# Optimization experiments

Hardware: AMD Instinct MI355X
Metric: run time of the kernel (lower is better)

The kernel has to match this reference:

```python
import jax, jax.numpy as jnp
from jax import lax
import jax.scipy.linalg as jsl
import numpy as np

R, N_MONTE, N_X = 8192, 64, 32


def _spd(a, n_x):
    # A @ A^T / n_x + I  -> well-conditioned SPD
    eye = jnp.eye(n_x, dtype=a.dtype)
    return jnp.einsum('...ij,...kj->...ik', a, a) / n_x + eye


def setup_inputs() -> dict:
    key = jax.random.key(0)
    k1, k2, k3, k4, k5 = jax.random.split(key, 5)
    x_hessian_diags = _spd(jax.random.normal(k1, (R, N_X, N_X), jnp.float32) * 0.5, N_X)
    x_grads = jax.random.normal(k2, (R, 1, N_X), jnp.float32) * 0.1
    x_trans_mat = jax.random.normal(k3, (N_X, N_X), jnp.float32) * (0.5 / np.sqrt(N_X))
    x_trans_prec = jnp.eye(N_X, dtype=jnp.float32)  # as in _compute_eta_loss_2
    x_init_prec = _spd(jax.random.normal(k4, (N_X, N_X), jnp.float32) * 0.5, N_X)
    epsx = jax.random.normal(k5, (R, N_MONTE, N_X), jnp.float32)
    return {
        'x_hessian_diags': x_hessian_diags,
        'x_grads': x_grads,
        'x_trans_mat': x_trans_mat,
        'x_trans_prec': x_trans_prec,
        'x_init_prec': x_init_prec,
        'epsx': epsx,
    }


def _cholesky_update(x_hessian_diags, x_grads, x_trans_mat, x_trans_prec, x_init_prec, epsx):
    r, n_monte, n_x = epsx.shape
    # A @ P @ A^T, constant across steps
    apat = x_trans_mat @ x_trans_prec @ x_trans_mat.T
    ap = x_trans_mat @ x_trans_prec
    # ms: 1 for all but the last step (last step has no successor coupling)
    ms = jnp.concatenate([jnp.ones(r - 1, x_hessian_diags.dtype), jnp.zeros(1, x_hessian_diags.dtype)])

    def fwd_step(carry, elem):
        pred_prec, off, u = carry  # [n_x,n_x], [n_x,n_x], [1,n_x]
        hess, grad, m = elem
        # block Cholesky diagonal factor
        chol = jnp.linalg.cholesky(pred_prec + hess + m * apat)
        # forward substitution for the mean rhs
        u = jsl.solve_triangular(chol, (grad - u @ off.T).T, lower=True).T
        # off-diagonal Cholesky block
        off = jsl.solve_triangular(chol, -ap, lower=True).T
        pred_prec = x_trans_prec - off @ off.T
        return (pred_prec, off, u), (chol, off, u)

    init = (x_init_prec, jnp.zeros((n_x, n_x), epsx.dtype), jnp.zeros((1, n_x), epsx.dtype))
    _, (chols, offs, us) = lax.scan(fwd_step, init, (x_hessian_diags, x_grads, ms))

    # backward substitution: smoothed mean (col 0) + posterior samples (cols 1:)
    gs = jnp.concatenate([us, epsx], axis=1)  # [R, 1+n_monte, n_x]

    def bwd_step(vw, elem):
        chol, off, g = elem
        vw = jsl.solve_triangular(chol.T, (g - vw @ off).T, lower=False).T
        return vw, vw

    _, vws = lax.scan(bwd_step, jnp.zeros((n_monte + 1, n_x), epsx.dtype), (chols, offs, gs), reverse=True)
    vs, ws = vws[:, :1], vws[:, 1:]
    return chols, offs, vs, ws


def reference(x_hessian_diags, x_grads, x_trans_mat, x_trans_prec, x_init_prec, epsx):
    _, _, vs, ws = _cholesky_update(x_hessian_diags, x_grads, x_trans_mat, x_trans_prec, x_init_prec, epsx)
    # x_tilde = vs + ws as consumed by _compute_eta_loss_2 (broadcast over n_monte)
    return vs + ws  # [R, n_monte, n_x]
```

## Files before the change

kernel.cpp:

```cpp
#include <hip/hip_runtime.h>
#include <hip/hip_bf16.h>

#define R_TOT 8192
#define NX 32
#define NM 64
#define STRD 33
#define VSTRD 36
#define OPSTRD 36
#define WARMF 8
#define WARMB 8
#define CHUNKF 4
#define CHUNKB 16

#define PIDX(k) ((((k) & 1) << 4) | ((k) >> 1))

__device__ inline void wsync() { asm volatile("s_waitcnt lgkmcnt(0)" ::: "memory"); }

__device__ inline float rdlane(float v, int l) {
  return __uint_as_float(__builtin_amdgcn_readlane(__float_as_uint(v), l));
}

__device__ inline unsigned f2bf(float x) {
  unsigned u = __float_as_uint(x);
  return (u + 0x7fffu + ((u >> 16) & 1u)) >> 16;
}

__device__ inline void st16(float* g, const float* v) {
  float4* p = reinterpret_cast<float4*>(g);
  p[0] = make_float4(v[0], v[1], v[2], v[3]);
  p[1] = make_float4(v[4], v[5], v[6], v[7]);
  p[2] = make_float4(v[8], v[9], v[10], v[11]);
  p[3] = make_float4(v[12], v[13], v[14], v[15]);
}
__device__ inline void st16(__hip_bfloat16* g, const float* v) {
  unsigned w[8];
  #pragma unroll
  for (int q = 0; q < 8; ++q)
    w[q] = (f2bf(v[2*q+1]) << 16) | f2bf(v[2*q]);
  uint4* p = reinterpret_cast<uint4*>(g);
  p[0] = make_uint4(w[0], w[1], w[2], w[3]);
  p[1] = make_uint4(w[4], w[5], w[6], w[7]);
}

__device__ inline void ld4(float* v, const float* g) {
  float4 a = *reinterpret_cast<const float4*>(g);
  v[0] = a.x; v[1] = a.y; v[2] = a.z; v[3] = a.w;
}
__device__ inline void ld4(float* v, const __hip_bfloat16* g) {
  uint2 a = *reinterpret_cast<const uint2*>(g);
  v[0] = __uint_as_float(a.x << 16);
  v[1] = __uint_as_float(a.x & 0xffff0000u);
  v[2] = __uint_as_float(a.y << 16);
  v[3] = __uint_as_float(a.y & 0xffff0000u);
}

__global__ __launch_bounds__(64) void precomp_kernel(
    const float* __restrict__ A, const float* __restrict__ P,
    float* __restrict__ apG, float* __restrict__ apatG)
{
  __shared__ float As[NX*STRD], Ps[NX*STRD], aps[NX*STRD];
  const int t = threadIdx.x;
  for (int e = t; e < NX*NX; e += 64) {
    int i = e >> 5, j = e & 31;
    As[i*STRD+j] = A[e];
    Ps[i*STRD+j] = P[e];
  }
  wsync();
  for (int e = t; e < NX*NX; e += 64) {
    int i = e >> 5, j = e & 31;
    float s = 0.f;
    for (int k = 0; k < NX; ++k) s += As[i*STRD+k] * Ps[k*STRD+j];
    aps[i*STRD+j] = s;
    apG[e] = s;
  }
  wsync();
  for (int e = t; e < NX*NX; e += 64) {
    int i = e >> 5, j = e & 31;
    float s = 0.f;
    for (int k = 0; k < NX; ++k) s += aps[i*STRD+k] * As[j*STRD+k];
    apatG[e] = s;
  }
}

template<typename ST>
__global__ __launch_bounds__(64, 2) void fwd_kernel(
    const float* __restrict__ hessAll, const float* __restrict__ gradAll,
    const float* __restrict__ apG, const float* __restrict__ apatG,
    const float* __restrict__ P, const float* __restrict__ initP,
    ST* __restrict__ offOut, ST* __restrict__ xOut, float* __restrict__ uOut)
{
  __shared__ float apP[NX*32], smx[NX*STRD], offP[NX*OPSTRD];
  __shared__ float uv[NX], tv[NX];
  const int t = threadIdx.x;
  const int lane = t & 31, half = t >> 5;
  const int pl = PIDX(lane);
  const int c = blockIdx.x;
  const int r0 = c * CHUNKF, r1 = r0 + CHUNKF;

  float PsR[16], apatR[16], predR[16], hessR[16];
  float gradR;

  const int cl = 16*(lane & 1) + (lane >> 1);
  #pragma unroll
  for (int m = 0; m < 16; ++m) {
    int e = t + 64*m;
    apP[(half + 2*m)*32 + cl] = apG[e];
    PsR[m]   = P[e];
    apatR[m] = apatG[e];
  }
  for (int e = t; e < NX*OPSTRD; e += 64) offP[e] = 0.f;
  wsync();

  int rstart = r0 - WARMF;
  if (rstart < 0) rstart = 0;
  const bool exact = (rstart == 0);

  #pragma unroll
  for (int m = 0; m < 16; ++m)
    predR[m] = exact ? initP[t + 64*m] : PsR[m];
  if (t < NX) uv[t] = 0.f;
  wsync();

  {
    const float* hess = hessAll + (size_t)rstart * (NX*NX);
    #pragma unroll
    for (int m = 0; m < 16; ++m) hessR[m] = hess[t + 64*m];
    gradR = gradAll[(size_t)rstart * NX + lane];
  }

  for (int r = rstart; r < r1; ++r) {
    const bool last = (r == R_TOT-1);
    #pragma unroll
    for (int m = 0; m < 16; ++m) {
      float v = predR[m] + hessR[m];
      if (!last) v += apatR[m];
      smx[(half + 2*m)*STRD + lane] = v;
    }
    wsync();
    if (r + 1 < r1) {
      const float* hn = hessAll + (size_t)(r+1) * (NX*NX);
      #pragma unroll
      for (int m = 0; m < 16; ++m) hessR[m] = hn[t + 64*m];
    }
    float row[NX];
    #pragma unroll
    for (int k = 0; k < NX; ++k) row[k] = smx[lane*STRD + k];
    #pragma unroll
    for (int j = 0; j < NX-1; ++j) {
      float invd = __builtin_amdgcn_rcpf(rdlane(row[j], j));
      float f = (lane > j) ? row[j] * invd : 0.f;
      #pragma unroll
      for (int cc = j+1; cc < NX; ++cc)
        row[cc] = fmaf(-f, rdlane(row[cc], j), row[cc]);
    }
    float zc[NX];
    #pragma unroll
    for (int i = 0; i < NX; ++i) {
      float d_i = rdlane(row[i], i);
      float di = __builtin_amdgcn_rcpf(d_i);
      float s = 0.f;
      #pragma unroll
      for (int k = 0; k < i; ++k) s = fmaf(rdlane(row[k], i), zc[k], s);
      zc[i] = (i == lane) ? di : -di * s;
    }
    #pragma unroll
    for (int i = 0; i < NX; ++i)
      zc[i] *= __builtin_amdgcn_sqrtf(rdlane(row[i], i));
    if (t < NX) {
      #pragma unroll
      for (int i = 0; i < NX; ++i) smx[i*STRD + t] = zc[i];
      if (r >= r0) {
        ST* xp = xOut + (size_t)r * (NX*NX) + t*NX;
        st16(xp, zc);
        st16(xp + 16, zc + 16);
      }
    }
    wsync();
    if (t < NX) {
      float s = gradR;
      #pragma unroll 4
      for (int m = 0; m < NX; ++m) s -= uv[m] * offP[m*OPSTRD + pl];
      tv[t] = s;
    }
    wsync();
    float unew = 0.f;
    if (t < NX) {
      float s = 0.f;
      #pragma unroll 4
      for (int k = 0; k < NX; ++k) s += tv[k] * smx[t*STRD+k];
      unew = s;
    }
    wsync();
    if (t < NX) {
      uv[t] = unew;
      if (r >= r0) uOut[(size_t)r*NX + t] = unew;
    }
    if (r + 1 < r1) gradR = gradAll[(size_t)(r+1) * NX + lane];
    wsync();
    {
      float offR[16];
      #pragma unroll
      for (int m = 0; m < 16; ++m) offR[m] = 0.f;
      #pragma unroll
      for (int k = 0; k < NX; ++k) {
        float xv = smx[lane*STRD + k];
        const float4* apv = reinterpret_cast<const float4*>(&apP[k*32 + 16*half]);
        float4 a0 = apv[0], a1 = apv[1], a2 = apv[2], a3 = apv[3];
        offR[0]  = fmaf(-xv, a0.x, offR[0]);  offR[1]  = fmaf(-xv, a0.y, offR[1]);
        offR[2]  = fmaf(-xv, a0.z, offR[2]);  offR[3]  = fmaf(-xv, a0.w, offR[3]);
        offR[4]  = fmaf(-xv, a1.x, offR[4]);  offR[5]  = fmaf(-xv, a1.y, offR[5]);
        offR[6]  = fmaf(-xv, a1.z, offR[6]);  offR[7]  = fmaf(-xv, a1.w, offR[7]);
        offR[8]  = fmaf(-xv, a2.x, offR[8]);  offR[9]  = fmaf(-xv, a2.y, offR[9]);
        offR[10] = fmaf(-xv, a2.z, offR[10]); offR[11] = fmaf(-xv, a2.w, offR[11]);
        offR[12] = fmaf(-xv, a3.x, offR[12]); offR[13] = fmaf(-xv, a3.y, offR[13]);
        offR[14] = fmaf(-xv, a3.z, offR[14]); offR[15] = fmaf(-xv, a3.w, offR[15]);
      }
      float4* opw = reinterpret_cast<float4*>(&offP[lane*OPSTRD + 16*half]);
      opw[0] = make_float4(offR[0],  offR[1],  offR[2],  offR[3]);
      opw[1] = make_float4(offR[4],  offR[5],  offR[6],  offR[7]);
      opw[2] = make_float4(offR[8],  offR[9],  offR[10], offR[11]);
      opw[3] = make_float4(offR[12], offR[13], offR[14], offR[15]);
      if (r >= r0)
        st16(offOut + (size_t)r * (NX*NX) + lane*NX + 16*half, offR);
    }
    wsync();
    #pragma unroll
    for (int m = 0; m < 16; ++m) predR[m] = PsR[m];
    #pragma unroll
    for (int k = 0; k < NX; ++k) {
      float fj = offP[k*OPSTRD + pl];
      const float4* ov = reinterpret_cast<const float4*>(&offP[k*OPSTRD + 16*half]);
      float4 o0 = ov[0], o1 = ov[1], o2 = ov[2], o3 = ov[3];
      predR[0]  -= o0.x*fj; predR[1]  -= o0.y*fj; predR[2]  -= o0.z*fj; predR[3]  -= o0.w*fj;
      predR[4]  -= o1.x*fj; predR[5]  -= o1.y*fj; predR[6]  -= o1.z*fj; predR[7]  -= o1.w*fj;
      predR[8]  -= o2.x*fj; predR[9]  -= o2.y*fj; predR[10] -= o2.z*fj; predR[11] -= o2.w*fj;
      predR[12] -= o3.x*fj; predR[13] -= o3.y*fj; predR[14] -= o3.z*fj; predR[15] -= o3.w*fj;
    }
    wsync();
  }
}

template<typename ST>
__global__ __launch_bounds__(256, 4) void bwd_kernel(
    const ST* __restrict__ offIn, const ST* __restrict__ xIn, const float* __restrict__ uIn,
    const float* __restrict__ epsx, float* __restrict__ outp)
{
  __shared__ float vw[(NM+1)*VSTRD], bb[(NM+1)*VSTRD], off[NX*STRD], xi[NX*STRD];
  const int t = threadIdx.x;
  const int lane = t & 31, grp = t >> 5;
  const int col = t >> 3, sg = t & 7;
  const int c = blockIdx.x;
  const int r0 = c * CHUNKB, r1 = r0 + CHUNKB;
  int rstart = r1 + WARMB; if (rstart > R_TOT) rstart = R_TOT;
  const bool has64 = (grp == 0);

  for (int e = t; e < (NM+1)*VSTRD; e += 256) vw[e] = 0.f;

  float ov[4], xv[4], gR[9];
  {
    int r = rstart - 1;
    size_t sb = (size_t)r * (NX*NX) + col*NX + 4*sg;
    ld4(ov, offIn + sb);
    ld4(xv, xIn + sb);
    const float* eps_r = epsx + (size_t)r * (NM*NX);
    const float* u_r   = uIn + (size_t)r * NX;
    #pragma unroll
    for (int m = 0; m < 8; ++m) {
      int i = grp + 8*m;
      gR[m] = (i == 0) ? u_r[lane] : eps_r[(i-1)*NX + lane];
    }
    gR[8] = has64 ? eps_r[63*NX + lane] : 0.f;
  }
  __syncthreads();

  for (int r = rstart - 1; r >= r0; --r) {
    float acc[9];
    #pragma unroll
    for (int m = 0; m < 9; ++m) acc[m] = gR[m];
    #pragma unroll
    for (int q = 0; q < 4; ++q) {
      int s = 4*sg + q;
      int io = ((s >> 4) & 1) | ((s & 15) << 1);
      off[io*STRD + col] = ov[q];
      xi[s*STRD + col]   = xv[q];
    }
    __syncthreads();
    if (r > r0) {
      size_t sb = (size_t)(r-1) * (NX*NX) + col*NX + 4*sg;
      ld4(ov, offIn + sb);
      ld4(xv, xIn + sb);
      const float* eps_n = epsx + (size_t)(r-1) * (NM*NX);
      const float* u_n   = uIn + (size_t)(r-1) * NX;
      #pragma unroll
      for (int m = 0; m < 8; ++m) {
        int i = grp + 8*m;
        gR[m] = (i == 0) ? u_n[lane] : eps_n[(i-1)*NX + lane];
      }
      if (has64) gR[8] = eps_n[63*NX + lane];
    }
    {
      float fo[NX];
      #pragma unroll
      for (int k = 0; k < NX; ++k) fo[k] = off[k*STRD + lane];
      #pragma unroll
      for (int m = 0; m < 8; ++m) {
        const float4* vr = reinterpret_cast<const float4*>(&vw[(grp + 8*m)*VSTRD]);
        #pragma unroll
        for (int q = 0; q < 8; ++q) {
          float4 v4 = vr[q];
          acc[m] -= v4.x*fo[4*q] + v4.y*fo[4*q+1] + v4.z*fo[4*q+2] + v4.w*fo[4*q+3];
        }
      }
      if (has64) {
        const float4* vr = reinterpret_cast<const float4*>(&vw[64*VSTRD]);
        #pragma unroll
        for (int q = 0; q < 8; ++q) {
          float4 v4 = vr[q];
          acc[8] -= v4.x*fo[4*q] + v4.y*fo[4*q+1] + v4.z*fo[4*q+2] + v4.w*fo[4*q+3];
        }
      }
    }
    #pragma unroll
    for (int m = 0; m < 8; ++m) bb[(grp + 8*m)*VSTRD + lane] = acc[m];
    if (has64) bb[64*VSTRD + lane] = acc[8];
    __syncthreads();
    float vacc[9];
    #pragma unroll
    for (int m = 0; m < 9; ++m) vacc[m] = 0.f;
    {
      float fx[NX];
      #pragma unroll
      for (int k = 0; k < NX; ++k) fx[k] = xi[k*STRD + lane];
      #pragma unroll
      for (int m = 0; m < 8; ++m) {
        const float4* br = reinterpret_cast<const float4*>(&bb[(grp + 8*m)*VSTRD]);
        #pragma unroll
        for (int q = 0; q < 8; ++q) {
          float4 b4 = br[q];
          vacc[m] += b4.x*fx[4*q] + b4.y*fx[4*q+1] + b4.z*fx[4*q+2] + b4.w*fx[4*q+3];
        }
      }
      if (has64) {
        const float4* br = reinterpret_cast<const float4*>(&bb[64*VSTRD]);
        #pragma unroll
        for (int q = 0; q < 8; ++q) {
          float4 b4 = br[q];
          vacc[8] += b4.x*fx[4*q] + b4.y*fx[4*q+1] + b4.z*fx[4*q+2] + b4.w*fx[4*q+3];
        }
      }
    }
    #pragma unroll
    for (int m = 0; m < 8; ++m) vw[(grp + 8*m)*VSTRD + lane] = vacc[m];
    if (has64) vw[64*VSTRD + lane] = vacc[8];
    __syncthreads();
    if (r < r1) {
      float v0 = vw[lane];
      float* out_r = outp + (size_t)r * (NM*NX);
      #pragma unroll
      for (int m = 0; m < 8; ++m)
        out_r[(grp + 8*m)*NX + lane] = vw[(grp + 8*m + 1)*VSTRD + lane] + v0;
    }
  }
}

extern "C" void kernel_launch(void* const* d_in, const int* in_sizes, int n_in,
                              void* d_out, int out_size, void* d_ws, size_t ws_size,
                              hipStream_t stream) {
  const float* hess  = (const float*)d_in[0];
  const float* grads = (const float*)d_in[1];
  const float* A     = (const float*)d_in[2];
  const float* P     = (const float*)d_in[3];
  const float* initP = (const float*)d_in[4];
  const float* epsx  = (const float*)d_in[5];
  float* outp = (float*)d_out;

  const size_t mats = (size_t)R_TOT * NX * NX;
  const size_t uN   = (size_t)R_TOT * NX;
  const size_t needF32 = 2ull * mats * sizeof(float) + uN * sizeof(float) + 2048 * sizeof(float);

  if (ws_size >= needF32) {
    float* offS  = (float*)d_ws;
    float* xS    = offS + mats;
    float* uS    = xS + mats;
    float* apG   = uS + uN;
    float* apatG = apG + 1024;
    precomp_kernel<<<dim3(1), dim3(64), 0, stream>>>(A, P, apG, apatG);
    fwd_kernel<float><<<dim3(R_TOT/CHUNKF), dim3(64), 0, stream>>>(
        hess, grads, apG, apatG, P, initP, offS, xS, uS);
    bwd_kernel<float><<<dim3(R_TOT/CHUNKB), dim3(256), 0, stream>>>(
        offS, xS, uS, epsx, outp);
  } else {
    __hip_bfloat16* offS = (__hip_bfloat16*)d_ws;
    __hip_bfloat16* xS   = offS + mats;
    float* uS            = (float*)(xS + mats);
    float* apG           = uS + uN;
    float* apatG         = apG + 1024;
    precomp_kernel<<<dim3(1), dim3(64), 0, stream>>>(A, P, apG, apatG);
    fwd_kernel<__hip_bfloat16><<<dim3(R_TOT/CHUNKF), dim3(64), 0, stream>>>(
        hess, grads, apG, apatG, P, initP, offS, xS, uS);
    bwd_kernel<__hip_bfloat16><<<dim3(R_TOT/CHUNKB), dim3(256), 0, stream>>>(
        offS, xS, uS, epsx, outp);
  }
}
```

Baseline: 470.6 us.

## Compute inverse Cholesky factor directly via elimination on identity rows

Replaces the two-phase approach (in-register LDL-style elimination of the matrix, then a separate triangular inversion) with a single sweep that builds the inverse factor row by row. Each step recomputes a pivot row as a dot product of the working rows with the original matrix columns, then eliminates. The output is stored transposed, and the backward kernel's indexing for xi is adjusted to match. The loops are kept rolled (unroll 1) and split so the first half only updates 16 columns, trading more readlane dot products per step for less code and lower register pressure.

```diff
diff --git a/kernel.cpp b/kernel.cpp
--- a/kernel.cpp
+++ b/kernel.cpp
@@ -142,37 +142,50 @@
       #pragma unroll
       for (int m = 0; m < 16; ++m) hessR[m] = hn[t + 64*m];
     }
-    float row[NX];
-    #pragma unroll
-    for (int k = 0; k < NX; ++k) row[k] = smx[lane*STRD + k];
-    #pragma unroll
-    for (int j = 0; j < NX-1; ++j) {
-      float invd = __builtin_amdgcn_rcpf(rdlane(row[j], j));
-      float f = (lane > j) ? row[j] * invd : 0.f;
-      #pragma unroll
-      for (int cc = j+1; cc < NX; ++cc)
-        row[cc] = fmaf(-f, rdlane(row[cc], j), row[cc]);
-    }
-    float zc[NX];
-    #pragma unroll
-    for (int i = 0; i < NX; ++i) {
-      float d_i = rdlane(row[i], i);
-      float di = __builtin_amdgcn_rcpf(d_i);
-      float s = 0.f;
-      #pragma unroll
-      for (int k = 0; k < i; ++k) s = fmaf(rdlane(row[k], i), zc[k], s);
-      zc[i] = (i == lane) ? di : -di * s;
-    }
-    #pragma unroll
-    for (int i = 0; i < NX; ++i)
-      zc[i] *= __builtin_amdgcn_sqrtf(rdlane(row[i], i));
+    float s0c[NX], wr[NX];
+    #pragma unroll
+    for (int k = 0; k < NX; ++k) s0c[k] = smx[k*STRD + lane];
+    #pragma unroll
+    for (int k = 0; k < NX; ++k) wr[k] = (k == lane) ? 1.f : 0.f;
+    float dsave = 1.f;
+    #pragma unroll 1
+    for (int j = 0; j < 16; ++j) {
+      float rowj = 0.f;
+      #pragma unroll
+      for (int k = 0; k < NX; ++k)
+        rowj = fmaf(wr[k], rdlane(s0c[k], j), rowj);
+      float dj = rdlane(rowj, j);
+      dsave = (j == lane) ? rowj : dsave;
+      float f = (lane > j) ? rowj * __builtin_amdgcn_rcpf(dj) : 0.f;
+      #pragma unroll
+      for (int cc = 0; cc < 16; ++cc)
+        wr[cc] = fmaf(-f, rdlane(wr[cc], j), wr[cc]);
+    }
+    #pragma unroll 1
+    for (int j = 16; j < NX; ++j) {
+      float rowj = 0.f;
+      #pragma unroll
+      for (int k = 0; k < NX; ++k)
+        rowj = fmaf(wr[k], rdlane(s0c[k], j), rowj);
+      float dj = rdlane(rowj, j);
+      dsave = (j == lane) ? rowj : dsave;
+      float f = (lane > j) ? rowj * __builtin_amdgcn_rcpf(dj) : 0.f;
+      #pragma unroll
+      for (int cc = 0; cc < NX; ++cc)
+        wr[cc] = fmaf(-f, rdlane(wr[cc], j), wr[cc]);
+    }
+    {
+      float rsd = __builtin_amdgcn_rcpf(__builtin_amdgcn_sqrtf(dsave));
+      #pragma unroll
+      for (int cc = 0; cc < NX; ++cc) wr[cc] *= rsd;
+    }
     if (t < NX) {
       #pragma unroll
-      for (int i = 0; i < NX; ++i) smx[i*STRD + t] = zc[i];
+      for (int cc = 0; cc < NX; ++cc) smx[lane*STRD + cc] = wr[cc];
       if (r >= r0) {
-        ST* xp = xOut + (size_t)r * (NX*NX) + t*NX;
-        st16(xp, zc);
-        st16(xp + 16, zc + 16);
+        ST* xp = xOut + (size_t)r * (NX*NX) + lane*NX;
+        st16(xp, wr);
+        st16(xp + 16, wr + 16);
       }
     }
     wsync();
@@ -282,7 +295,7 @@
       int s = 4*sg + q;
       int io = ((s >> 4) & 1) | ((s & 15) << 1);
       off[io*STRD + col] = ov[q];
-      xi[s*STRD + col]   = xv[q];
+      xi[col*STRD + s]   = xv[q];
     }
     __syncthreads();
     if (r > r0) {
```

Result: slower. 570.0 us (+21.1%).
